# Kernel tuning notes

Hardware: AMD Instinct MI355X
Metric: run time of the kernel (lower is better)

The kernel has to match this reference:

```python
import jax, jax.numpy as jnp
import numpy as np

B, S, D, H = 8, 1024, 768, 12
HD = D // H  # head_dim = 64


def setup_inputs() -> dict:
    key = jax.random.key(0)
    ks = jax.random.split(key, 9)
    s = 0.02
    return {
        "hidden_states": jax.random.normal(ks[0], (B, S, D), dtype=jnp.float32),
        "Wq": jax.random.normal(ks[1], (D, D), dtype=jnp.float32) * s,
        "bq": jnp.zeros((D,), dtype=jnp.float32),
        "Wk": jax.random.normal(ks[2], (D, D), dtype=jnp.float32) * s,
        "bk": jnp.zeros((D,), dtype=jnp.float32),
        "Wv": jax.random.normal(ks[3], (D, D), dtype=jnp.float32) * s,
        "bv": jnp.zeros((D,), dtype=jnp.float32),
        "Wo": jax.random.normal(ks[4], (D, D), dtype=jnp.float32) * s,
        "bo": jnp.zeros((D,), dtype=jnp.float32),
    }


def reference(hidden_states, Wq, bq, Wk, bk, Wv, bv, Wo, bo):
    b, s, d = hidden_states.shape
    scale = 1.0 / jnp.sqrt(jnp.asarray(HD, dtype=hidden_states.dtype))
    # projections (weights stored as [in, out])
    q = hidden_states @ Wq + bq
    k = hidden_states @ Wk + bk
    v = hidden_states @ Wv + bv
    # [B, H, S, HD]
    q = q.reshape(b, s, H, HD).transpose(0, 2, 1, 3)
    k = k.reshape(b, s, H, HD).transpose(0, 2, 1, 3)
    v = v.reshape(b, s, H, HD).transpose(0, 2, 1, 3)
    # explicit O(S^2) attention, matching the original unfused math
    attn = jnp.einsum("bhqd,bhkd->bhqk", q, k) * scale
    attn = jax.nn.softmax(attn, axis=-1)
    out = jnp.einsum("bhqk,bhkd->bhqd", attn, v)
    out = out.transpose(0, 2, 1, 3).reshape(b, s, d)
    return out @ Wo + bo
```

## Files before the change

### kernel.cpp

```cpp
#include <hip/hip_runtime.h>
#include <stdint.h>

#define DEV __device__ __forceinline__

typedef __attribute__((ext_vector_type(8))) short bf16x8;
typedef __attribute__((ext_vector_type(4))) float f32x4;

#define MFMA16(a,b,c) __builtin_amdgcn_mfma_f32_16x16x32_bf16((a),(b),(c),0,0,0)

DEV unsigned short f2bf(float x){
  union { float f; unsigned u; } v; v.f = x;
  unsigned r = v.u + 0x7fffu + ((v.u >> 16) & 1u);
  return (unsigned short)(r >> 16);
}
DEV unsigned pack2(float a, float b){
  return (unsigned)f2bf(a) | ((unsigned)f2bf(b) << 16);
}
DEV bf16x8 mk_bf16x8(unsigned w0, unsigned w1, unsigned w2, unsigned w3){
  union { uint4 u; bf16x8 v; } cv;
  cv.u = make_uint4(w0, w1, w2, w3);
  return cv.v;
}

__global__ void cast_x_kernel(const float* __restrict__ x, uint4* __restrict__ out){
  int i = blockIdx.x * 256 + threadIdx.x;
  const float4* p = (const float4*)x + (size_t)i * 2;
  float4 a = p[0], b = p[1];
  out[i] = make_uint4(pack2(a.x,a.y), pack2(a.z,a.w), pack2(b.x,b.y), pack2(b.z,b.w));
}

__global__ void trans_w_kernel(const float* __restrict__ W0, const float* __restrict__ W1,
                               const float* __restrict__ W2, const float* __restrict__ W3,
                               unsigned short* __restrict__ T0, unsigned short* __restrict__ T1,
                               unsigned short* __restrict__ T2, unsigned short* __restrict__ T3){
  const float* W; unsigned short* T;
  switch (blockIdx.z) {
    case 0:  W = W0; T = T0; break;
    case 1:  W = W1; T = T1; break;
    case 2:  W = W2; T = T2; break;
    default: W = W3; T = T3; break;
  }
  __shared__ float tile[32][33];
  const int i0 = blockIdx.y * 32, o0 = blockIdx.x * 32;
  const int t = threadIdx.x;
  const int ir = t >> 3, oc = (t & 7) * 4;
  float4 v = *(const float4*)(W + (size_t)(i0 + ir) * 768 + o0 + oc);
  tile[ir][oc+0] = v.x; tile[ir][oc+1] = v.y; tile[ir][oc+2] = v.z; tile[ir][oc+3] = v.w;
  __syncthreads();
  const int orow = t >> 3, ic = (t & 7) * 4;
  uint2 w;
  w.x = pack2(tile[ic+0][orow], tile[ic+1][orow]);
  w.y = pack2(tile[ic+2][orow], tile[ic+3][orow]);
  *(uint2*)(T + (size_t)(o0 + orow) * 768 + i0 + ic) = w;
}

__launch_bounds__(256, 4)
__global__ void gemm_qkv(const unsigned short* __restrict__ Wcat,
                         const unsigned short* __restrict__ X16,
                         const float* __restrict__ bq, const float* __restrict__ bk,
                         const float* __restrict__ bv,
                         unsigned short* __restrict__ Qb, unsigned short* __restrict__ Kb,
                         unsigned short* __restrict__ VTb)
{
  __shared__ __align__(16) unsigned char lds[4][8192];
  const int lane = threadIdx.x & 63, wid = threadIdx.x >> 6;
  const int lin = blockIdx.x;
  const int nid = (lin & 7) * 144 + (lin >> 3);
  const int m0 = (nid % 18) * 128;
  const int n0 = (nid / 18) * 128;
  const int wm = wid >> 1, wn = wid & 1;

  f32x4 acc[4][4] = {};

  for (int t = 0; t < 24; ++t) {
    const int buf = t & 1;
    const int k0 = t * 32;
    #pragma unroll
    for (int i = 0; i < 2; ++i) {
      const int c   = i * 256 + wid * 64 + lane;
      const int row = ((c >> 6) << 4) + (c & 15);
      const int kk  = ((c >> 4) & 3) * 8;
      const unsigned short* sa = Wcat + (size_t)(m0 + row) * 768 + k0 + kk;
      const unsigned short* sb = X16  + (size_t)(n0 + row) * 768 + k0 + kk;
      __builtin_amdgcn_global_load_lds(
          (const __attribute__((address_space(1))) void*)sa,
          (__attribute__((address_space(3))) void*)&lds[buf][(i * 256 + wid * 64) * 16],
          16, 0, 0);
      __builtin_amdgcn_global_load_lds(
          (const __attribute__((address_space(1))) void*)sb,
          (__attribute__((address_space(3))) void*)&lds[2 + buf][(i * 256 + wid * 64) * 16],
          16, 0, 0);
    }
    __syncthreads();

    bf16x8 afr[4], bfr[4];
    #pragma unroll
    for (int mb = 0; mb < 4; ++mb)
      afr[mb] = *(const bf16x8*)&lds[buf][((wm * 4 + mb) * 64 + lane) * 16];
    #pragma unroll
    for (int nb = 0; nb < 4; ++nb)
      bfr[nb] = *(const bf16x8*)&lds[2 + buf][((wn * 4 + nb) * 64 + lane) * 16];
    #pragma unroll
    for (int mb = 0; mb < 4; ++mb)
      #pragma unroll
      for (int nb = 0; nb < 4; ++nb)
        acc[mb][nb] = MFMA16(afr[mb], bfr[nb], acc[mb][nb]);
  }

  const int l15 = lane & 15, lg = lane >> 4;
  const int sel = m0 / 768;
  const int mbase = m0 - sel * 768;
  #pragma unroll
  for (int mb = 0; mb < 4; ++mb) {
    #pragma unroll
    for (int nb = 0; nb < 4; ++nb) {
      const int rowl = wm * 64 + mb * 16 + lg * 4;
      const int coll = wn * 64 + nb * 16 + l15;
      f32x4 a = acc[mb][nb];
      const int chan = mbase + rowl;
      const int sg   = n0 + coll;
      const int b = sg >> 10, s = sg & 1023, h = chan >> 6, hd = chan & 63;
      if (sel != 2) {
        float4 bi = *(const float4*)((sel == 0 ? bq : bk) + chan);
        uint2 w;
        w.x = pack2(a[0] + bi.x, a[1] + bi.y);
        w.y = pack2(a[2] + bi.z, a[3] + bi.w);
        unsigned short* o = (sel == 0 ? Qb : Kb);
        *(uint2*)(o + ((size_t)(b * 12 + h) * 1024 + s) * 64 + hd) = w;
      } else {
        float4 bi = *(const float4*)(bv + chan);
        size_t base = ((size_t)(b * 12 + h) * 64 + hd) * 1024 + s;
        VTb[base       ] = f2bf(a[0] + bi.x);
        VTb[base + 1024] = f2bf(a[1] + bi.y);
        VTb[base + 2048] = f2bf(a[2] + bi.z);
        VTb[base + 3072] = f2bf(a[3] + bi.w);
      }
    }
  }
}

__launch_bounds__(256, 3)
__global__ void gemm_out(const unsigned short* __restrict__ matA,
                         const unsigned short* __restrict__ matB,
                         float* __restrict__ outp,
                         const float* __restrict__ bias)
{
  __shared__ __align__(16) unsigned char ldsA[2][4096];
  __shared__ __align__(16) unsigned char ldsB[2][8192];
  const int lane = threadIdx.x & 63, wid = threadIdx.x >> 6;
  const int lin = blockIdx.x;
  const int nid = (lin & 7) * 96 + (lin >> 3);
  const int m0 = (nid % 12) * 64;
  const int n0 = (nid / 12) * 128;
  const int wm = wid >> 1, wn = wid & 1;

  f32x4 acc[2][4] = {};

  for (int t = 0; t < 24; ++t) {
    const int buf = t & 1;
    const int k0 = t * 32;
    {
      const int c   = wid * 64 + lane;
      const int row = ((c >> 6) << 4) + (c & 15);
      const int kk  = ((c >> 4) & 3) * 8;
      const unsigned short* sa = matA + (size_t)(m0 + row) * 768 + k0 + kk;
      __builtin_amdgcn_global_load_lds(
          (const __attribute__((address_space(1))) void*)sa,
          (__attribute__((address_space(3))) void*)&ldsA[buf][c * 16], 16, 0, 0);
    }
    #pragma unroll
    for (int i = 0; i < 2; ++i) {
      const int c   = i * 256 + wid * 64 + lane;
      const int row = ((c >> 6) << 4) + (c & 15);
      const int kk  = ((c >> 4) & 3) * 8;
      const unsigned short* sb = matB + (size_t)(n0 + row) * 768 + k0 + kk;
      __builtin_amdgcn_global_load_lds(
          (const __attribute__((address_space(1))) void*)sb,
          (__attribute__((address_space(3))) void*)&ldsB[buf][c * 16], 16, 0, 0);
    }
    __syncthreads();

    bf16x8 afr[2], bfr[4];
    #pragma unroll
    for (int mb = 0; mb < 2; ++mb)
      afr[mb] = *(const bf16x8*)&ldsA[buf][((wm * 2 + mb) * 64 + lane) * 16];
    #pragma unroll
    for (int nb = 0; nb < 4; ++nb)
      bfr[nb] = *(const bf16x8*)&ldsB[buf][((wn * 4 + nb) * 64 + lane) * 16];
    #pragma unroll
    for (int mb = 0; mb < 2; ++mb)
      #pragma unroll
      for (int nb = 0; nb < 4; ++nb)
        acc[mb][nb] = MFMA16(afr[mb], bfr[nb], acc[mb][nb]);
  }

  const int l15 = lane & 15, lg = lane >> 4;
  #pragma unroll
  for (int mb = 0; mb < 2; ++mb) {
    #pragma unroll
    for (int nb = 0; nb < 4; ++nb) {
      const int rowl = wm * 32 + mb * 16 + lg * 4;
      const int coll = wn * 64 + nb * 16 + l15;
      f32x4 a = acc[mb][nb];
      int chan = m0 + rowl, sg = n0 + coll;
      float4 bi = *(const float4*)(bias + chan);
      float4 o = make_float4(a[0] + bi.x, a[1] + bi.y, a[2] + bi.z, a[3] + bi.w);
      *(float4*)(outp + (size_t)sg * 768 + chan) = o;
    }
  }
}

__launch_bounds__(256, 4)
__global__ void attn_kernel(const unsigned short* __restrict__ Q,
                            const unsigned short* __restrict__ K,
                            const unsigned short* __restrict__ VT,
                            unsigned short* __restrict__ AO)
{
  __shared__ __align__(16) unsigned char kbuf[8192];
  __shared__ __align__(16) unsigned char vbuf[8192];
  const int lane = threadIdx.x & 63, wid = threadIdx.x >> 6;
  const int l15 = lane & 15, lg = lane >> 4;
  const int bh = blockIdx.x;
  const int q0 = blockIdx.y * 128 + wid * 32;
  const unsigned short* Qp = Q  + (size_t)bh * 65536;
  const unsigned short* Kp = K  + (size_t)bh * 65536;
  const unsigned short* Vp = VT + (size_t)bh * 65536;

  bf16x8 qf[2][2];
  #pragma unroll
  for (int f = 0; f < 2; ++f)
    #pragma unroll
    for (int kc = 0; kc < 2; ++kc)
      qf[f][kc] = *(const bf16x8*)(Qp + (size_t)(q0 + f * 16 + l15) * 64 + kc * 32 + lg * 8);

  f32x4 acco[2][4] = {};
  float lsum[2] = {0.f, 0.f};

  const int src0 = l15 + ((lg & 1) << 5);
  const int src1 = src0 + 16;
  const bool hi = (lg & 2) != 0;

  for (int t = 0; t < 16; ++t) {
    const int kv0 = t * 64;
    #pragma unroll
    for (int i = 0; i < 2; ++i) {
      const int g = wid * 2 + i;
      const unsigned short* sk = Kp + (size_t)(kv0 + (g >> 1) * 16 + l15) * 64 + (g & 1) * 32 + lg * 8;
      __builtin_amdgcn_global_load_lds(
          (const __attribute__((address_space(1))) void*)sk,
          (__attribute__((address_space(3))) void*)&kbuf[g * 1024], 16, 0, 0);
      const unsigned short* sv = Vp + (size_t)((g >> 1) * 16 + l15) * 1024 + kv0 + (g & 1) * 32 + lg * 8;
      __builtin_amdgcn_global_load_lds(
          (const __attribute__((address_space(1))) void*)sv,
          (__attribute__((address_space(3))) void*)&vbuf[g * 1024], 16, 0, 0);
    }
    __syncthreads();

    f32x4 sc[2][4] = {};
    #pragma unroll
    for (int mb = 0; mb < 4; ++mb) {
      #pragma unroll
      for (int kc = 0; kc < 2; ++kc) {
        bf16x8 kf = *(const bf16x8*)&kbuf[((mb * 2 + kc) * 64 + lane) * 16];
        sc[0][mb] = MFMA16(kf, qf[0][kc], sc[0][mb]);
        sc[1][mb] = MFMA16(kf, qf[1][kc], sc[1][mb]);
      }
    }
    unsigned p01[2][4], p23[2][4];
    #pragma unroll
    for (int f = 0; f < 2; ++f) {
      float sum = 0.f;
      #pragma unroll
      for (int mb = 0; mb < 4; ++mb) {
        float e0 = __expf(sc[f][mb][0] * 0.125f);
        float e1 = __expf(sc[f][mb][1] * 0.125f);
        float e2 = __expf(sc[f][mb][2] * 0.125f);
        float e3 = __expf(sc[f][mb][3] * 0.125f);
        sum += (e0 + e1) + (e2 + e3);
        p01[f][mb] = pack2(e0, e1);
        p23[f][mb] = pack2(e2, e3);
      }
      sum += __shfl_xor(sum, 16);
      sum += __shfl_xor(sum, 32);
      lsum[f] += sum;
    }
    bf16x8 pf[2][2];
    #pragma unroll
    for (int f = 0; f < 2; ++f) {
      #pragma unroll
      for (int c = 0; c < 2; ++c) {
        unsigned a0 = __shfl(p01[f][2*c], src0), b0 = __shfl(p01[f][2*c+1], src0);
        unsigned a1 = __shfl(p23[f][2*c], src0), b1 = __shfl(p23[f][2*c+1], src0);
        unsigned a2 = __shfl(p01[f][2*c], src1), b2 = __shfl(p01[f][2*c+1], src1);
        unsigned a3 = __shfl(p23[f][2*c], src1), b3 = __shfl(p23[f][2*c+1], src1);
        pf[f][c] = mk_bf16x8(hi ? b0 : a0, hi ? b1 : a1, hi ? b2 : a2, hi ? b3 : a3);
      }
    }
    #pragma unroll
    for (int hb = 0; hb < 4; ++hb) {
      #pragma unroll
      for (int c = 0; c < 2; ++c) {
        bf16x8 vf = *(const bf16x8*)&vbuf[((hb * 2 + c) * 64 + lane) * 16];
        acco[0][hb] = MFMA16(vf, pf[0][c], acco[0][hb]);
        acco[1][hb] = MFMA16(vf, pf[1][c], acco[1][hb]);
      }
    }
    __syncthreads();
  }

  const int b = bh / 12, h = bh % 12;
  #pragma unroll
  for (int f = 0; f < 2; ++f) {
    const float rl = 1.0f / lsum[f];
    const int s = q0 + f * 16 + l15;
    const size_t base = ((size_t)(b * 1024 + s)) * 768 + h * 64;
    #pragma unroll
    for (int hb = 0; hb < 4; ++hb) {
      uint2 w;
      w.x = pack2(acco[f][hb][0] * rl, acco[f][hb][1] * rl);
      w.y = pack2(acco[f][hb][2] * rl, acco[f][hb][3] * rl);
      *(uint2*)(AO + base + hb * 16 + lg * 4) = w;
    }
  }
}

extern "C" void kernel_launch(void* const* d_in, const int* in_sizes, int n_in,
                              void* d_out, int out_size, void* d_ws, size_t ws_size,
                              hipStream_t stream)
{
  const float* hs = (const float*)d_in[0];
  const float* Wq = (const float*)d_in[1];
  const float* bq = (const float*)d_in[2];
  const float* Wk = (const float*)d_in[3];
  const float* bk = (const float*)d_in[4];
  const float* Wv = (const float*)d_in[5];
  const float* bv = (const float*)d_in[6];
  const float* Wo = (const float*)d_in[7];
  const float* bo = (const float*)d_in[8];

  const size_t SZ_X = (size_t)8192 * 768 * 2;
  const size_t SZ_W = (size_t)768 * 768 * 2;
  const size_t NEED = SZ_X * 5 + SZ_W * 4;
  if (ws_size < NEED) return;

  char* ws = (char*)d_ws;
  unsigned short* X16 = (unsigned short*)ws;
  unsigned short* Wqt = (unsigned short*)(ws + SZ_X);
  unsigned short* Wkt = Wqt + 768 * 768;
  unsigned short* Wvt = Wkt + 768 * 768;
  unsigned short* Wot = Wvt + 768 * 768;
  unsigned short* Qb  = (unsigned short*)(ws + SZ_X + 4 * SZ_W);
  unsigned short* Kb  = Qb  + (size_t)8192 * 768;
  unsigned short* VTb = Kb  + (size_t)8192 * 768;
  unsigned short* AOb = VTb + (size_t)8192 * 768;

  cast_x_kernel<<<dim3(3072), dim3(256), 0, stream>>>(hs, (uint4*)X16);
  trans_w_kernel<<<dim3(24, 24, 4), dim3(256), 0, stream>>>(Wq, Wk, Wv, Wo, Wqt, Wkt, Wvt, Wot);

  gemm_qkv<<<dim3(1152), dim3(256), 0, stream>>>(Wqt, X16, bq, bk, bv, Qb, Kb, VTb);

  attn_kernel<<<dim3(96, 8), dim3(256), 0, stream>>>(Qb, Kb, VTb, AOb);

  gemm_out<<<dim3(768), dim3(256), 0, stream>>>(Wot, AOb, (float*)d_out, bo);
}
```

Baseline: 174.5 us.

## Software-pipeline global-to-LDS loads two stages ahead in QKV and output GEMMs

Both projection GEMMs now prefetch the next K tile into the freed LDS buffer while the MFMAs for the current tile run. Partial vmcnt waits and explicit barriers replace the single __syncthreads after each load. This is meant to hide global load latency that the old loop exposed on every iteration. It adds an extra barrier per iteration and redundant loads of the last tile at the tail. It also relies on hand-counted vmcnt values being correct.

```diff
diff --git a/kernel.cpp b/kernel.cpp
--- a/kernel.cpp
+++ b/kernel.cpp
@@ -72,26 +72,34 @@
 
   f32x4 acc[4][4] = {};
 
+  #define QKV_STAGE(BUF, TT)                                                        \
+    {                                                                               \
+      const int k0s = (TT) * 32;                                                    \
+      _Pragma("unroll")                                                             \
+      for (int i = 0; i < 2; ++i) {                                                 \
+        const int c   = i * 256 + wid * 64 + lane;                                  \
+        const int row = ((c >> 6) << 4) + (c & 15);                                 \
+        const int kk  = ((c >> 4) & 3) * 8;                                         \
+        const unsigned short* sa = Wcat + (size_t)(m0 + row) * 768 + k0s + kk;      \
+        const unsigned short* sb = X16  + (size_t)(n0 + row) * 768 + k0s + kk;      \
+        __builtin_amdgcn_global_load_lds(                                           \
+            (const __attribute__((address_space(1))) void*)sa,                      \
+            (__attribute__((address_space(3))) void*)&lds[BUF][(i*256+wid*64)*16],  \
+            16, 0, 0);                                                              \
+        __builtin_amdgcn_global_load_lds(                                           \
+            (const __attribute__((address_space(1))) void*)sb,                      \
+            (__attribute__((address_space(3))) void*)&lds[2+(BUF)][(i*256+wid*64)*16], \
+            16, 0, 0);                                                              \
+      }                                                                             \
+    }
+
+  QKV_STAGE(0, 0)
+  QKV_STAGE(1, 1)
+
   for (int t = 0; t < 24; ++t) {
     const int buf = t & 1;
-    const int k0 = t * 32;
-    #pragma unroll
-    for (int i = 0; i < 2; ++i) {
-      const int c   = i * 256 + wid * 64 + lane;
-      const int row = ((c >> 6) << 4) + (c & 15);
-      const int kk  = ((c >> 4) & 3) * 8;
-      const unsigned short* sa = Wcat + (size_t)(m0 + row) * 768 + k0 + kk;
-      const unsigned short* sb = X16  + (size_t)(n0 + row) * 768 + k0 + kk;
-      __builtin_amdgcn_global_load_lds(
-          (const __attribute__((address_space(1))) void*)sa,
-          (__attribute__((address_space(3))) void*)&lds[buf][(i * 256 + wid * 64) * 16],
-          16, 0, 0);
-      __builtin_amdgcn_global_load_lds(
-          (const __attribute__((address_space(1))) void*)sb,
-          (__attribute__((address_space(3))) void*)&lds[2 + buf][(i * 256 + wid * 64) * 16],
-          16, 0, 0);
-    }
-    __syncthreads();
+    asm volatile("s_waitcnt vmcnt(4)" ::: "memory");
+    __builtin_amdgcn_s_barrier();
 
     bf16x8 afr[4], bfr[4];
     #pragma unroll
@@ -100,12 +108,20 @@
     #pragma unroll
     for (int nb = 0; nb < 4; ++nb)
       bfr[nb] = *(const bf16x8*)&lds[2 + buf][((wn * 4 + nb) * 64 + lane) * 16];
+
+    asm volatile("s_waitcnt lgkmcnt(0)" ::: "memory");
+    __builtin_amdgcn_s_barrier();
+
+    const int tt = (t + 2 < 24) ? (t + 2) : 23;
+    QKV_STAGE(buf, tt)
+
     #pragma unroll
     for (int mb = 0; mb < 4; ++mb)
       #pragma unroll
       for (int nb = 0; nb < 4; ++nb)
         acc[mb][nb] = MFMA16(afr[mb], bfr[nb], acc[mb][nb]);
   }
+  #undef QKV_STAGE
 
   const int l15 = lane & 15, lg = lane >> 4;
   const int sel = m0 / 768;
@@ -156,29 +172,37 @@
 
   f32x4 acc[2][4] = {};
 
+  #define OUT_STAGE(BUF, TT)                                                        \
+    {                                                                               \
+      const int k0s = (TT) * 32;                                                    \
+      {                                                                             \
+        const int c   = wid * 64 + lane;                                            \
+        const int row = ((c >> 6) << 4) + (c & 15);                                 \
+        const int kk  = ((c >> 4) & 3) * 8;                                         \
+        const unsigned short* sa = matA + (size_t)(m0 + row) * 768 + k0s + kk;      \
+        __builtin_amdgcn_global_load_lds(                                           \
+            (const __attribute__((address_space(1))) void*)sa,                      \
+            (__attribute__((address_space(3))) void*)&ldsA[BUF][c * 16], 16, 0, 0); \
+      }                                                                             \
+      _Pragma("unroll")                                                             \
+      for (int i = 0; i < 2; ++i) {                                                 \
+        const int c   = i * 256 + wid * 64 + lane;                                  \
+        const int row = ((c >> 6) << 4) + (c & 15);                                 \
+        const int kk  = ((c >> 4) & 3) * 8;                                         \
+        const unsigned short* sb = matB + (size_t)(n0 + row) * 768 + k0s + kk;      \
+        __builtin_amdgcn_global_load_lds(                                           \
+            (const __attribute__((address_space(1))) void*)sb,                      \
+            (__attribute__((address_space(3))) void*)&ldsB[BUF][c * 16], 16, 0, 0); \
+      }                                                                             \
+    }
+
+  OUT_STAGE(0, 0)
+  OUT_STAGE(1, 1)
+
   for (int t = 0; t < 24; ++t) {
     const int buf = t & 1;
-    const int k0 = t * 32;
-    {
-      const int c   = wid * 64 + lane;
-      const int row = ((c >> 6) << 4) + (c & 15);
-      const int kk  = ((c >> 4) & 3) * 8;
-      const unsigned short* sa = matA + (size_t)(m0 + row) * 768 + k0 + kk;
-      __builtin_amdgcn_global_load_lds(
-          (const __attribute__((address_space(1))) void*)sa,
-          (__attribute__((address_space(3))) void*)&ldsA[buf][c * 16], 16, 0, 0);
-    }
-    #pragma unroll
-    for (int i = 0; i < 2; ++i) {
-      const int c   = i * 256 + wid * 64 + lane;
-      const int row = ((c >> 6) << 4) + (c & 15);
-      const int kk  = ((c >> 4) & 3) * 8;
-      const unsigned short* sb = matB + (size_t)(n0 + row) * 768 + k0 + kk;
-      __builtin_amdgcn_global_load_lds(
-          (const __attribute__((address_space(1))) void*)sb,
-          (__attribute__((address_space(3))) void*)&ldsB[buf][c * 16], 16, 0, 0);
-    }
-    __syncthreads();
+    asm volatile("s_waitcnt vmcnt(3)" ::: "memory");
+    __builtin_amdgcn_s_barrier();
 
     bf16x8 afr[2], bfr[4];
     #pragma unroll
@@ -187,12 +211,20 @@
     #pragma unroll
     for (int nb = 0; nb < 4; ++nb)
       bfr[nb] = *(const bf16x8*)&ldsB[buf][((wn * 4 + nb) * 64 + lane) * 16];
+
+    asm volatile("s_waitcnt lgkmcnt(0)" ::: "memory");
+    __builtin_amdgcn_s_barrier();
+
+    const int tt = (t + 2 < 24) ? (t + 2) : 23;
+    OUT_STAGE(buf, tt)
+
     #pragma unroll
     for (int mb = 0; mb < 2; ++mb)
       #pragma unroll
       for (int nb = 0; nb < 4; ++nb)
         acc[mb][nb] = MFMA16(afr[mb], bfr[nb], acc[mb][nb]);
   }
+  #undef OUT_STAGE
 
   const int l15 = lane & 15, lg = lane >> 4;
   #pragma unroll
```

Result: slower. 188.4 us (+8.0%).
